# Optimization experiments

Hardware: AMD Instinct MI355X
Metric: run time of the kernel (lower is better)

Reference implementation:

```python
import jax, jax.numpy as jnp
import numpy as np
import math

B, S, D, H, DK, FF, L = 4, 1024, 512, 8, 64, 2048, 4
IN, NS, SD, TOPK = 768, 4, 64, 2


def _ln(x, g, b, eps=1e-5):
    mu = jnp.mean(x, -1, keepdims=True)
    var = jnp.mean((x - mu) ** 2, -1, keepdims=True)
    return (x - mu) / jnp.sqrt(var + eps) * g + b


def _pos_emb(s, d):
    pos = jnp.arange(s, dtype=jnp.float32)[:, None]
    div = jnp.exp(jnp.arange(0, d, 2, dtype=jnp.float32) * (-math.log(10000.0) / d))
    pe = jnp.zeros((s, d), jnp.float32)
    pe = pe.at[:, 0::2].set(jnp.sin(pos * div))
    pe = pe.at[:, 1::2].set(jnp.cos(pos * div))
    return pe


def setup_inputs() -> dict:
    key = jax.random.key(0)
    ks = iter(jax.random.split(key, 40))
    r = lambda *sh: jax.random.normal(next(ks), sh, jnp.float32)
    p = lambda *sh: jax.random.normal(next(ks), sh, jnp.float32) * 0.02
    inp = {
        'q_raw_seq': r(B, S, NS, IN),
        'm_seq': r(B, S, SD),
        'qa_embed': r(B, S, D),
        # MoE expert FFNs: Linear(IN,IN) -> ReLU -> Linear(IN,D)
        'exp_w1': p(NS, IN, IN), 'exp_b1': jnp.zeros((NS, IN)),
        'exp_w2': p(NS, IN, D), 'exp_b2': jnp.zeros((NS, D)),
        # router input adapter Linear(NS*IN, D)
        'adapt_w': p(NS * IN, D), 'adapt_b': jnp.zeros((D,)),
        'gate_w': p(D + SD, NS), 'gate_b': jnp.zeros((NS,)),
        'moe_ln_g': jnp.ones((D,)), 'moe_ln_b': jnp.zeros((D,)),
        # transformer blocks (kq_same=1 -> k_linear shared for q and k)
        'kw': p(L, D, D), 'kb': jnp.zeros((L, D)),
        'vw': p(L, D, D), 'vb': jnp.zeros((L, D)),
        'ow': p(L, D, D), 'ob': jnp.zeros((L, D)),
        'ln1_g': jnp.ones((L, D)), 'ln1_b': jnp.zeros((L, D)),
        'ff_w1': p(L, D, FF), 'ff_b1': jnp.zeros((L, FF)),
        'ff_w2': p(L, FF, D), 'ff_b2': jnp.zeros((L, D)),
        'ln2_g': jnp.ones((L, D)), 'ln2_b': jnp.zeros((L, D)),
    }
    return inp


def _forward(q_raw_seq, m_seq, qa_embed, exp_w1, exp_b1, exp_w2, exp_b2,
             adapt_w, adapt_b, gate_w, gate_b, moe_ln_g, moe_ln_b,
             kw, kb, vw, vb, ow, ob, ln1_g, ln1_b,
             ff_w1, ff_b1, ff_w2, ff_b2, ln2_g, ln2_b):
    # ---- PolyaParallelMoE (eval: no noise/dropout), has_stages=True ----
    h1 = jax.nn.relu(jnp.einsum('bske,kef->bskf', q_raw_seq, exp_w1) + exp_b1[None, None])
    experts = jnp.einsum('bskf,kfm->bskm', h1, exp_w2) + exp_b2[None, None]  # [B,S,4,D]
    q_flat = q_raw_seq.reshape(q_raw_seq.shape[0], q_raw_seq.shape[1], NS * IN)
    summary = jax.nn.relu(q_flat @ adapt_w + adapt_b)
    logits = jnp.concatenate([summary, m_seq], -1) @ gate_w + gate_b  # [B,S,4]
    top_vals, _ = jax.lax.top_k(logits, TOPK)
    thresh = top_vals[..., -1:]
    masked = jnp.where(logits >= thresh, logits, -jnp.inf)  # scatter top-k, -inf elsewhere
    gate_weights = jax.nn.softmax(masked, -1)
    combined = jnp.einsum('bskm,bsk->bsm', experts, gate_weights)
    q_embed = _ln(combined, moe_ln_g, moe_ln_b)

    # ---- Architecture: positional add + causal transformer blocks ----
    pe = _pos_emb(S, D)
    x = q_embed + pe
    y = qa_embed + pe
    allow = jnp.tril(jnp.ones((S, S), bool), -1)  # strict lower: np.triu(k=0)==0
    scale = 1.0 / math.sqrt(DK)
    for i in range(L):
        kh = (x @ kw[i] + kb[i]).reshape(B, S, H, DK).transpose(0, 2, 1, 3)
        vh = (y @ vw[i] + vb[i]).reshape(B, S, H, DK).transpose(0, 2, 1, 3)
        # kq_same: q = k_linear(query), query==key==x -> qh == kh
        scores = jnp.einsum('bhid,bhjd->bhij', kh, kh) * scale
        scores = jnp.where(allow, scores, -1e32)
        attn = jax.nn.softmax(scores, -1)
        attn = attn.at[:, :, 0, :].set(0.0)  # zero_pad first query row
        ctx = jnp.einsum('bhij,bhjd->bhid', attn, vh).transpose(0, 2, 1, 3).reshape(B, S, D)
        x = _ln(x + (ctx @ ow[i] + ob[i]), ln1_g[i], ln1_b[i])
        ffn = jax.nn.relu(x @ ff_w1[i] + ff_b1[i]) @ ff_w2[i] + ff_b2[i]
        x = _ln(x + ffn, ln2_g[i], ln2_b[i])
        y = x  # after first block, value stream follows torch loop (values=y fixed)
        y = qa_embed + pe  # values stay qa stream per Architecture.forward
    return x


def reference(q_raw_seq, m_seq, qa_embed, exp_w1, exp_b1, exp_w2, exp_b2,
              adapt_w, adapt_b, gate_w, gate_b, moe_ln_g, moe_ln_b,
              kw, kb, vw, vb, ow, ob, ln1_g, ln1_b,
              ff_w1, ff_b1, ff_w2, ff_b2, ln2_g, ln2_b):
    # NOTE: in Architecture.forward, each block is called with query=x, key=x, values=y
    # where y = qa_embed + pe stays fixed across blocks.
    def fwd(*a):
        return _forward(*a)
    return fwd(q_raw_seq, m_seq, qa_embed, exp_w1, exp_b1, exp_w2, exp_b2,
               adapt_w, adapt_b, gate_w, gate_b, moe_ln_g, moe_ln_b,
               kw, kb, vw, vb, ow, ob, ln1_g, ln1_b,
               ff_w1, ff_b1, ff_w2, ff_b2, ln2_g, ln2_b)
```

## Files before the change

### kernel.cpp

```cpp
#include <hip/hip_runtime.h>
#include <hip/hip_bf16.h>

typedef unsigned short u16;
typedef __attribute__((ext_vector_type(8))) short short8;
typedef __attribute__((ext_vector_type(4))) float floatx4;

template <typename T> struct is_u16 { static constexpr bool v = false; };
template <> struct is_u16<u16> { static constexpr bool v = true; };

__device__ __forceinline__ float bf2f(u16 u) {
    unsigned x = (unsigned)u << 16;
    return __uint_as_float(x);
}
__device__ __forceinline__ u16 f2bf(float f) {
    unsigned x = __float_as_uint(f);
    unsigned r = (x + 0x7fffu + ((x >> 16) & 1u)) >> 16;
    return (u16)r;
}

__device__ __forceinline__ float wave_sum(float v) {
    #pragma unroll
    for (int off = 32; off; off >>= 1) v += __shfl_xor(v, off);
    return v;
}

__device__ __forceinline__ void async16(const u16* g, const u16* lds) {
    __builtin_amdgcn_global_load_lds(
        (const __attribute__((address_space(1))) void*)g,
        (__attribute__((address_space(3))) void*)lds, 16, 0, 0);
}

__device__ __forceinline__ void hilo8(const float* p, u16* hi, u16* lo) {
    float4 a = *(const float4*)p, b = *(const float4*)(p + 4);
    float v[8] = {a.x, a.y, a.z, a.w, b.x, b.y, b.z, b.w};
    #pragma unroll
    for (int i = 0; i < 8; ++i) {
        u16 h = f2bf(v[i]);
        hi[i] = h;
        lo[i] = f2bf(v[i] - bf2f(h));
    }
}

__global__ __launch_bounds__(256) void hilo_conv_kernel(
    const float* __restrict__ in, u16* __restrict__ hi, u16* __restrict__ lo)
{
    const size_t i = ((size_t)blockIdx.x * 256 + threadIdx.x) * 8;
    u16 h[8], l[8];
    hilo8(in + i, h, l);
    *(uint4*)&hi[i] = *(const uint4*)h;
    *(uint4*)&lo[i] = *(const uint4*)l;
}

__device__ __forceinline__ void gemm_body(
    const u16* __restrict__ A, int lda,
    const u16* __restrict__ Bt, int ldb,
    const float* __restrict__ bias,
    float* __restrict__ Cf, u16* __restrict__ Cb, int ldc,
    int K, int act, int transC, int m0, int n0)
{
    __shared__ __align__(16) u16 Asm[2 * 128 * 32];
    __shared__ __align__(16) u16 Bsm[2 * 128 * 32];

    const int tid = threadIdx.x;
    const int lane = tid & 63;
    const int wave = tid >> 6;
    const int wm = (wave >> 1) * 64, wn = (wave & 1) * 64;

    const int r0 = tid >> 2;
    const int kc = (tid & 3) * 8;

    const int kq = (lane >> 4) * 8;
    const int fm = lane & 15;

    const floatx4 zz = {0.f, 0.f, 0.f, 0.f};
    floatx4 acc[4][4];
    #pragma unroll
    for (int mt = 0; mt < 4; ++mt)
        #pragma unroll
        for (int nt = 0; nt < 4; ++nt) acc[mt][nt] = zz;

    const u16* ldsA = Asm + wave * 512;
    const u16* ldsB = Bsm + wave * 512;

    for (int kt = 0; kt < K; kt += 64) {
        #pragma unroll
        for (int h = 0; h < 2; ++h) {
            async16(&A[(size_t)(m0 + r0) * lda + kt + h * 32 + kc],      ldsA + h * 4096);
            async16(&A[(size_t)(m0 + r0 + 64) * lda + kt + h * 32 + kc], ldsA + h * 4096 + 2048);
            async16(&Bt[(size_t)(n0 + r0) * ldb + kt + h * 32 + kc],      ldsB + h * 4096);
            async16(&Bt[(size_t)(n0 + r0 + 64) * ldb + kt + h * 32 + kc], ldsB + h * 4096 + 2048);
        }
        __syncthreads();

        #pragma unroll
        for (int h = 0; h < 2; ++h) {
            short8 af[4], bfr[4];
            #pragma unroll
            for (int mt = 0; mt < 4; ++mt)
                af[mt] = *(const short8*)&Asm[h * 4096 + (wm + mt * 16 + fm) * 32 + kq];
            #pragma unroll
            for (int nt = 0; nt < 4; ++nt)
                bfr[nt] = *(const short8*)&Bsm[h * 4096 + (wn + nt * 16 + fm) * 32 + kq];

            #pragma unroll
            for (int mt = 0; mt < 4; ++mt)
                #pragma unroll
                for (int nt = 0; nt < 4; ++nt)
                    acc[mt][nt] = __builtin_amdgcn_mfma_f32_16x16x32_bf16(
                        af[mt], bfr[nt], acc[mt][nt], 0, 0, 0);
        }
        __syncthreads();
    }

    const int cr = (lane >> 4) * 4;
    #pragma unroll
    for (int mt = 0; mt < 4; ++mt) {
        #pragma unroll
        for (int nt = 0; nt < 4; ++nt) {
            const int col = n0 + wn + nt * 16 + fm;
            const float bz = bias ? bias[col] : 0.f;
            #pragma unroll
            for (int r = 0; r < 4; ++r) {
                const int row = m0 + wm + mt * 16 + cr + r;
                float v = acc[mt][nt][r] + bz;
                if (act) v = fmaxf(v, 0.f);
                if (Cf) Cf[(size_t)row * ldc + col] = v;
                if (Cb) {
                    if (transC)
                        Cb[(((size_t)(row >> 10) * 512 + col) << 10) + (row & 1023)] = f2bf(v);
                    else
                        Cb[(size_t)row * ldc + col] = f2bf(v);
                }
            }
        }
    }
}

template <typename TA>
__global__ __launch_bounds__(256) void gemm_bf16(
    const TA* __restrict__ A, int lda, long strideAz,
    const u16* __restrict__ Bt, int ldb, long strideBz,
    const float* __restrict__ bias, int strideBiasZ,
    float* __restrict__ Cf, u16* __restrict__ Cb, int ldc, long strideCz,
    int K, int act, int transC, int NT)
{
    const int wg   = blockIdx.x;
    const int xcd  = wg & 7;
    const int slot = wg >> 3;
    const int nt   = slot % NT;
    const int pg   = slot / NT;
    const int panel = xcd + 8 * pg;
    const int my = panel & 31, mz = panel >> 5;

    A  += (size_t)mz * strideAz;
    Bt += (size_t)mz * strideBz;
    const float* bz = bias ? bias + (size_t)mz * strideBiasZ : nullptr;
    if (Cf) Cf += (size_t)mz * strideCz;
    if (Cb) Cb += (size_t)mz * strideCz;
    gemm_body(A, lda, Bt, ldb, bz, Cf, Cb, ldc, K, act, transC, my * 128, nt * 128);
}

__global__ __launch_bounds__(256) void gemm_kv(
    const u16* __restrict__ xb, const u16* __restrict__ yb,
    const u16* __restrict__ kwt, const u16* __restrict__ vwt,
    const float* __restrict__ kb, const float* __restrict__ vb,
    u16* __restrict__ khb, u16* __restrict__ vhT)
{
    const int wg   = blockIdx.x;
    const int xcd  = wg & 7;
    const int slot = wg >> 3;
    const int nt   = slot & 3;
    const int pg   = slot >> 2;
    const int panel = xcd + 8 * pg;
    const int my = panel & 31, mz = panel >> 5;

    if (mz == 0)
        gemm_body(xb, 512, kwt, 512, kb, nullptr, khb, 512, 512, 0, 0, my * 128, nt * 128);
    else
        gemm_body(yb, 512, vwt, 512, vb, nullptr, vhT, 512, 512, 0, 1, my * 128, nt * 128);
}

__global__ __launch_bounds__(256) void gemm_f32split(
    const u16* __restrict__ Ah, const u16* __restrict__ Al, int lda,
    const u16* __restrict__ Bh, const u16* __restrict__ Bl, int ldb,
    float* __restrict__ Cf, int ldc, long strideCz,
    int kz)
{
    __shared__ __align__(16) u16 Ahs[2 * 128 * 32];
    __shared__ __align__(16) u16 Als[2 * 128 * 32];
    __shared__ __align__(16) u16 Bhs[2 * 128 * 32];
    __shared__ __align__(16) u16 Bls[2 * 128 * 32];

    const int wg   = blockIdx.x;
    const int xcd  = wg & 7;
    const int slot = wg >> 3;
    const int nt4  = slot & 3;
    const int g    = xcd + 8 * (slot >> 2);
    const int my   = g & 31, mz = g >> 5;

    const int tid = threadIdx.x;
    const int lane = tid & 63;
    const int wave = tid >> 6;
    const int m0 = my * 128, n0 = nt4 * 128;
    const int wm = (wave >> 1) * 64, wn = (wave & 1) * 64;
    const int k0 = mz * kz;
    Cf += (size_t)mz * strideCz;

    const int r0 = tid >> 2;
    const int kc = (tid & 3) * 8;
    const int kq = (lane >> 4) * 8;
    const int fm = lane & 15;

    const floatx4 zz = {0.f, 0.f, 0.f, 0.f};
    floatx4 acc[4][4];
    #pragma unroll
    for (int mt = 0; mt < 4; ++mt)
        #pragma unroll
        for (int nt = 0; nt < 4; ++nt) acc[mt][nt] = zz;

    const u16* ldsAh = Ahs + wave * 512;
    const u16* ldsAl = Als + wave * 512;
    const u16* ldsBh = Bhs + wave * 512;
    const u16* ldsBl = Bls + wave * 512;

    for (int kt = 0; kt < kz; kt += 64) {
        #pragma unroll
        for (int h = 0; h < 2; ++h) {
            const size_t ka = (size_t)(m0 + r0) * lda + k0 + kt + h * 32 + kc;
            const size_t kb = (size_t)(n0 + r0) * ldb + k0 + kt + h * 32 + kc;
            async16(&Ah[ka],                     ldsAh + h * 4096);
            async16(&Ah[ka + (size_t)64 * lda],  ldsAh + h * 4096 + 2048);
            async16(&Al[ka],                     ldsAl + h * 4096);
            async16(&Al[ka + (size_t)64 * lda],  ldsAl + h * 4096 + 2048);
            async16(&Bh[kb],                     ldsBh + h * 4096);
            async16(&Bh[kb + (size_t)64 * ldb],  ldsBh + h * 4096 + 2048);
            async16(&Bl[kb],                     ldsBl + h * 4096);
            async16(&Bl[kb + (size_t)64 * ldb],  ldsBl + h * 4096 + 2048);
        }
        __syncthreads();

        #pragma unroll
        for (int h = 0; h < 2; ++h) {
            short8 ah[4], al[4], bh[4], bl[4];
            #pragma unroll
            for (int mt = 0; mt < 4; ++mt) {
                ah[mt] = *(const short8*)&Ahs[h * 4096 + (wm + mt * 16 + fm) * 32 + kq];
                al[mt] = *(const short8*)&Als[h * 4096 + (wm + mt * 16 + fm) * 32 + kq];
            }
            #pragma unroll
            for (int nt = 0; nt < 4; ++nt) {
                bh[nt] = *(const short8*)&Bhs[h * 4096 + (wn + nt * 16 + fm) * 32 + kq];
                bl[nt] = *(const short8*)&Bls[h * 4096 + (wn + nt * 16 + fm) * 32 + kq];
            }

            #pragma unroll
            for (int mt = 0; mt < 4; ++mt)
                #pragma unroll
                for (int nt = 0; nt < 4; ++nt) {
                    acc[mt][nt] = __builtin_amdgcn_mfma_f32_16x16x32_bf16(
                        ah[mt], bh[nt], acc[mt][nt], 0, 0, 0);
                    acc[mt][nt] = __builtin_amdgcn_mfma_f32_16x16x32_bf16(
                        al[mt], bh[nt], acc[mt][nt], 0, 0, 0);
                    acc[mt][nt] = __builtin_amdgcn_mfma_f32_16x16x32_bf16(
                        ah[mt], bl[nt], acc[mt][nt], 0, 0, 0);
                }
        }
        __syncthreads();
    }

    const int cr = (lane >> 4) * 4;
    #pragma unroll
    for (int mt = 0; mt < 4; ++mt) {
        #pragma unroll
        for (int nt = 0; nt < 4; ++nt) {
            const int col = n0 + wn + nt * 16 + fm;
            #pragma unroll
            for (int r = 0; r < 4; ++r) {
                const int row = m0 + wm + mt * 16 + cr + r;
                Cf[(size_t)row * ldc + col] = acc[mt][nt][r];
            }
        }
    }
}

__global__ __launch_bounds__(64) void gate_fused_kernel(
    const float* __restrict__ ps, const float* __restrict__ adapt_b,
    const float* __restrict__ m_seq,
    const float* __restrict__ gw, const float* __restrict__ gb,
    float* __restrict__ gates)
{
    const int r = blockIdx.x, t = threadIdx.x;
    float p0 = 0.f, p1 = 0.f, p2 = 0.f, p3 = 0.f;
    const float* pr = ps + (size_t)r * 512;
    for (int j = t; j < 512; j += 64) {
        float v = pr[j] + pr[j + 2097152] + pr[j + 4194304] + pr[j + 6291456] + adapt_b[j];
        float s = fmaxf(v, 0.f);
        const float* g = gw + (size_t)j * 4;
        p0 += s * g[0]; p1 += s * g[1]; p2 += s * g[2]; p3 += s * g[3];
    }
    {
        float m = m_seq[(size_t)r * 64 + t];
        const float* g = gw + (size_t)(512 + t) * 4;
        p0 += m * g[0]; p1 += m * g[1]; p2 += m * g[2]; p3 += m * g[3];
    }
    p0 = wave_sum(p0); p1 = wave_sum(p1); p2 = wave_sum(p2); p3 = wave_sum(p3);
    if (t == 0) {
        float lg[4] = { p0 + gb[0], p1 + gb[1], p2 + gb[2], p3 + gb[3] };
        float m1 = -INFINITY, m2 = -INFINITY;
        #pragma unroll
        for (int k = 0; k < 4; ++k) {
            float v = lg[k];
            if (v > m1) { m2 = m1; m1 = v; }
            else if (v > m2) { m2 = v; }
        }
        float wv[4], s = 0.f;
        #pragma unroll
        for (int k = 0; k < 4; ++k) {
            wv[k] = (lg[k] >= m2) ? __expf(lg[k] - m1) : 0.f;
            s += wv[k];
        }
        float inv = 1.f / s;
        #pragma unroll
        for (int k = 0; k < 4; ++k) gates[(size_t)r * 4 + k] = wv[k] * inv;
    }
}

__global__ __launch_bounds__(256) void tconv_kernel(
    const float* __restrict__ in, u16* __restrict__ out, int K, int N)
{
    __shared__ float t[32][33];
    const int n0 = blockIdx.x * 32, k0 = blockIdx.y * 32;
    const size_t bo = (size_t)blockIdx.z * K * N;
    const int tx = threadIdx.x & 31, ty = threadIdx.x >> 5;
    const float* src = in + bo;
    u16* dst = out + bo;
    #pragma unroll
    for (int r = ty; r < 32; r += 8) t[r][tx] = src[(size_t)(k0 + r) * N + n0 + tx];
    __syncthreads();
    #pragma unroll
    for (int r = ty; r < 32; r += 8) dst[(size_t)(n0 + r) * K + k0 + tx] = f2bf(t[tx][r]);
}

__global__ __launch_bounds__(256) void tconv3_kernel(
    const float* __restrict__ kw, const float* __restrict__ vw, const float* __restrict__ ow,
    u16* __restrict__ kwt, u16* __restrict__ vwt, u16* __restrict__ owt)
{
    __shared__ float t[32][33];
    const int z = blockIdx.z;
    const int sel = z >> 2, li = z & 3;
    const float* in = (sel == 0) ? kw : (sel == 1) ? vw : ow;
    u16* outp = (sel == 0) ? kwt : (sel == 1) ? vwt : owt;
    const size_t bo = (size_t)li * 262144;
    const int n0 = blockIdx.x * 32, k0 = blockIdx.y * 32;
    const int tx = threadIdx.x & 31, ty = threadIdx.x >> 5;
    const float* src = in + bo;
    u16* dst = outp + bo;
    #pragma unroll
    for (int r = ty; r < 32; r += 8) t[r][tx] = src[(size_t)(k0 + r) * 512 + n0 + tx];
    __syncthreads();
    #pragma unroll
    for (int r = ty; r < 32; r += 8) dst[(size_t)(n0 + r) * 512 + k0 + tx] = f2bf(t[tx][r]);
}

__global__ __launch_bounds__(256) void tconv_hilo_kernel(
    const float* __restrict__ in, u16* __restrict__ outh, u16* __restrict__ outl,
    int K, int N)
{
    __shared__ float t[32][33];
    const int n0 = blockIdx.x * 32, k0 = blockIdx.y * 32;
    const int tx = threadIdx.x & 31, ty = threadIdx.x >> 5;
    #pragma unroll
    for (int r = ty; r < 32; r += 8) t[r][tx] = in[(size_t)(k0 + r) * N + n0 + tx];
    __syncthreads();
    #pragma unroll
    for (int r = ty; r < 32; r += 8) {
        float v = t[tx][r];
        u16 h = f2bf(v);
        outh[(size_t)(n0 + r) * K + k0 + tx] = h;
        outl[(size_t)(n0 + r) * K + k0 + tx] = f2bf(v - bf2f(h));
    }
}

__global__ void pe_kernel(float* __restrict__ pe)
{
    int idx = blockIdx.x * 256 + threadIdx.x;
    int s = idx >> 9, d = idx & 511;
    float div = expf((float)(d & ~1) * (-9.210340371976184f / 512.0f));
    float ang = (float)s * div;
    pe[idx] = (d & 1) ? cosf(ang) : sinf(ang);
}

__global__ __launch_bounds__(64) void moe_ln_kernel(
    const u16* __restrict__ experts, const float* __restrict__ gates,
    const float* __restrict__ g, const float* __restrict__ bb,
    const float* __restrict__ pe, const float* __restrict__ qa,
    float* __restrict__ x, u16* __restrict__ xb, u16* __restrict__ yb)
{
    const int r = blockIdx.x, t = threadIdx.x;
    const u16* e = experts + (size_t)r * 2048;
    const float g0 = gates[r * 4 + 0], g1 = gates[r * 4 + 1];
    const float g2 = gates[r * 4 + 2], g3 = gates[r * 4 + 3];
    float v[8];
    #pragma unroll
    for (int it = 0; it < 8; ++it) {
        int d = t + it * 64;
        v[it] = g0 * bf2f(e[d]) + g1 * bf2f(e[512 + d])
              + g2 * bf2f(e[1024 + d]) + g3 * bf2f(e[1536 + d]);
    }
    float s = 0.f;
    #pragma unroll
    for (int it = 0; it < 8; ++it) s += v[it];
    s = wave_sum(s);
    const float mu = s * (1.f / 512.f);
    float q = 0.f;
    #pragma unroll
    for (int it = 0; it < 8; ++it) { float dd = v[it] - mu; q += dd * dd; }
    q = wave_sum(q);
    const float rstd = rsqrtf(q * (1.f / 512.f) + 1e-5f);
    const float* per = pe + (size_t)(r & 1023) * 512;
    #pragma unroll
    for (int it = 0; it < 8; ++it) {
        int d = t + it * 64;
        float pv = per[d];
        float o = (v[it] - mu) * rstd * g[d] + bb[d] + pv;
        x[(size_t)r * 512 + d] = o;
        xb[(size_t)r * 512 + d] = f2bf(o);
        yb[(size_t)r * 512 + d] = f2bf(qa[(size_t)r * 512 + d] + pv);
    }
}

__global__ __launch_bounds__(64) void add_ln_kernel(
    float* __restrict__ x, u16* __restrict__ xb,
    const float* __restrict__ t0, const float* __restrict__ t1,
    const float* __restrict__ bias,
    const float* __restrict__ g, const float* __restrict__ bb,
    float* __restrict__ out2)
{
    const int r = blockIdx.x, t = threadIdx.x;
    float* xr = x + (size_t)r * 512;
    float v[8];
    #pragma unroll
    for (int it = 0; it < 8; ++it) {
        int d = t + it * 64;
        float tv = t0[(size_t)r * 512 + d];
        if (t1) tv += t1[(size_t)r * 512 + d];
        if (bias) tv += bias[d];
        v[it] = xr[d] + tv;
    }
    float s = 0.f;
    #pragma unroll
    for (int it = 0; it < 8; ++it) s += v[it];
    s = wave_sum(s);
    const float mu = s * (1.f / 512.f);
    float q = 0.f;
    #pragma unroll
    for (int it = 0; it < 8; ++it) { float dd = v[it] - mu; q += dd * dd; }
    q = wave_sum(q);
    const float rstd = rsqrtf(q * (1.f / 512.f) + 1e-5f);
    #pragma unroll
    for (int it = 0; it < 8; ++it) {
        int d = t + it * 64;
        float o = (v[it] - mu) * rstd * g[d] + bb[d];
        xr[d] = o;
        xb[(size_t)r * 512 + d] = f2bf(o);
        if (out2) out2[(size_t)r * 512 + d] = o;
    }
}

__global__ __launch_bounds__(256) void attn_kernel(
    const u16* __restrict__ kh, const u16* __restrict__ vhT,
    u16* __restrict__ ctx)
{
    __shared__ __align__(16) u16 Qs[64 * 64];
    __shared__ __align__(16) u16 Ks[64 * 64];
    __shared__ __align__(16) u16 Vt[64 * 72];
    __shared__ __align__(16) u16 Ps[64 * 72];

    const int tid = threadIdx.x;
    const int lane = tid & 63, wave = tid >> 6;
    const int quad = lane >> 4, fm = lane & 15;
    const int b = blockIdx.x, h = blockIdx.y;
    const int bz = blockIdx.z;
    const int it = (bz < 8) ? bz : (23 - bz);

    const u16* khb = kh + ((size_t)b * 1024) * 512 + h * 64;
    const u16* vtb = vhT + ((size_t)(b * 512 + h * 64)) * 1024;

    const int lj = tid >> 2;
    const int lc = tid & 3;

    {
        const u16* src = khb + (size_t)(it * 64 + lj) * 512 + lc * 16;
        *(uint4*)&Qs[lj * 64 + lc * 16]     = *(const uint4*)src;
        *(uint4*)&Qs[lj * 64 + lc * 16 + 8] = *(const uint4*)(src + 8);
    }

    const floatx4 zz = {0.f, 0.f, 0.f, 0.f};
    floatx4 o_acc[4];
    #pragma unroll
    for (int nt = 0; nt < 4; ++nt) o_acc[nt] = zz;
    float m_run[4] = { -INFINITY, -INFINITY, -INFINITY, -INFINITY };
    float l_run[4] = {};

    __syncthreads();

    for (int jt = 0; jt <= it; ++jt) {
        {
            const u16* ksrc = khb + (size_t)(jt * 64 + lj) * 512 + lc * 16;
            *(uint4*)&Ks[lj * 64 + lc * 16]     = *(const uint4*)ksrc;
            *(uint4*)&Ks[lj * 64 + lc * 16 + 8] = *(const uint4*)(ksrc + 8);
            const u16* vsrc = vtb + (size_t)lj * 1024 + jt * 64 + lc * 16;
            *(uint4*)&Vt[lj * 72 + lc * 16]     = *(const uint4*)vsrc;
            *(uint4*)&Vt[lj * 72 + lc * 16 + 8] = *(const uint4*)(vsrc + 8);
        }
        __syncthreads();

        floatx4 s_acc[4];
        #pragma unroll
        for (int nt = 0; nt < 4; ++nt) s_acc[nt] = zz;
        #pragma unroll
        for (int ks = 0; ks < 2; ++ks) {
            short8 af = *(const short8*)&Qs[(wave * 16 + fm) * 64 + ks * 32 + quad * 8];
            #pragma unroll
            for (int nt = 0; nt < 4; ++nt) {
                short8 bf = *(const short8*)&Ks[(nt * 16 + fm) * 64 + ks * 32 + quad * 8];
                s_acc[nt] = __builtin_amdgcn_mfma_f32_16x16x32_bf16(af, bf, s_acc[nt], 0, 0, 0);
            }
        }

        const bool diag = (jt == it);
        #pragma unroll
        for (int r = 0; r < 4; ++r) {
            const int rowi = wave * 16 + quad * 4 + r;
            float sv[4];
            #pragma unroll
            for (int nt = 0; nt < 4; ++nt) {
                float s = s_acc[nt][r] * 0.125f;
                if (diag && (nt * 16 + fm) >= rowi) s = -INFINITY;
                sv[nt] = s;
            }
            float mx = fmaxf(fmaxf(sv[0], sv[1]), fmaxf(sv[2], sv[3]));
            #pragma unroll
            for (int off = 1; off < 16; off <<= 1) mx = fmaxf(mx, __shfl_xor(mx, off));
            const float mn = fmaxf(m_run[r], mx);
            const float mfix = (mn == -INFINITY) ? 0.f : mn;
            const float alpha = (m_run[r] == -INFINITY) ? 0.f : __expf(m_run[r] - mn);
            m_run[r] = mn;
            float rs = 0.f;
            #pragma unroll
            for (int nt = 0; nt < 4; ++nt) {
                float p = __expf(sv[nt] - mfix);
                Ps[rowi * 72 + nt * 16 + fm] = f2bf(p);
                rs += p;
            }
            #pragma unroll
            for (int off = 1; off < 16; off <<= 1) rs += __shfl_xor(rs, off);
            l_run[r] = l_run[r] * alpha + rs;
            #pragma unroll
            for (int nt = 0; nt < 4; ++nt) o_acc[nt][r] *= alpha;
        }
        __syncthreads();

        #pragma unroll
        for (int ks = 0; ks < 2; ++ks) {
            short8 af = *(const short8*)&Ps[(wave * 16 + fm) * 72 + ks * 32 + quad * 8];
            #pragma unroll
            for (int nt = 0; nt < 4; ++nt) {
                short8 bf = *(const short8*)&Vt[(nt * 16 + fm) * 72 + ks * 32 + quad * 8];
                o_acc[nt] = __builtin_amdgcn_mfma_f32_16x16x32_bf16(af, bf, o_acc[nt], 0, 0, 0);
            }
        }
        __syncthreads();
    }

    u16* cb = ctx + ((size_t)b * 1024 + (size_t)it * 64 + wave * 16) * 512 + h * 64;
    #pragma unroll
    for (int r = 0; r < 4; ++r) {
        const int row = quad * 4 + r;
        const float inv = (l_run[r] > 0.f) ? 1.f / l_run[r] : 0.f;
        #pragma unroll
        for (int nt = 0; nt < 4; ++nt)
            cb[(size_t)row * 512 + nt * 16 + fm] = f2bf(o_acc[nt][r] * inv);
    }
}

extern "C" void kernel_launch(void* const* d_in, const int* in_sizes, int n_in,
                              void* d_out, int out_size, void* d_ws, size_t ws_size,
                              hipStream_t stream)
{
    const float* q_raw   = (const float*)d_in[0];
    const float* m_seq   = (const float*)d_in[1];
    const float* qa      = (const float*)d_in[2];
    const float* exp_w1  = (const float*)d_in[3];
    const float* exp_b1  = (const float*)d_in[4];
    const float* exp_w2  = (const float*)d_in[5];
    const float* exp_b2  = (const float*)d_in[6];
    const float* adapt_w = (const float*)d_in[7];
    const float* adapt_b = (const float*)d_in[8];
    const float* gate_w  = (const float*)d_in[9];
    const float* gate_b  = (const float*)d_in[10];
    const float* moe_g   = (const float*)d_in[11];
    const float* moe_b   = (const float*)d_in[12];
    const float* kw      = (const float*)d_in[13];
    const float* kb      = (const float*)d_in[14];
    const float* vw      = (const float*)d_in[15];
    const float* vb      = (const float*)d_in[16];
    const float* ow      = (const float*)d_in[17];
    const float* ob      = (const float*)d_in[18];
    const float* ln1g    = (const float*)d_in[19];
    const float* ln1b    = (const float*)d_in[20];
    const float* fw1     = (const float*)d_in[21];
    const float* fb1     = (const float*)d_in[22];
    const float* fw2     = (const float*)d_in[23];
    const float* fb2     = (const float*)d_in[24];
    const float* ln2g    = (const float*)d_in[25];
    const float* ln2b    = (const float*)d_in[26];
    float* out = (float*)d_out;

    const size_t NEED = 125829120ull;
    if (ws_size < NEED) return;

    char* base = (char*)d_ws;
    float* x  = (float*)(base + 0);
    u16*  xb  = (u16*)(base + 8388608);
    u16*  yb  = (u16*)(base + 12582912);
    char* G = base + 16777216;
    u16*   w1t     = (u16*)(G + 0);
    u16*   w2t     = (u16*)(G + 4718592);
    float* psum    = (float*)(G + 7864320);
    u16*   h1b4    = (u16*)(G + 7864320);
    u16*   expb    = (u16*)(G + 33030144);
    float* pe      = (float*)(G + 49807360);
    float* gates   = (float*)(G + 51904512);
    u16*   adwh    = (u16*)(G + 52428800);
    u16*   adwl    = (u16*)(G + 55574528);
    u16*   qhi     = (u16*)(G + 58720256);
    u16*   qlo     = (u16*)(G + 83886080);
    u16*   kwt  = (u16*)(G + 0);
    u16*   vwt  = (u16*)(G + 2097152);
    u16*   owt  = (u16*)(G + 4194304);
    u16*   fw1t = (u16*)(G + 6291456);
    u16*   fw2t = (u16*)(G + 14680064);
    u16*   khb  = (u16*)(G + 23068672);
    u16*   vhT  = (u16*)(G + 27262976);
    u16*   ctxb = (u16*)(G + 31457280);
    float* p    = (float*)(G + 35651584);
    u16*   ffhb = (u16*)(G + 44040192);
    float* ps0  = (float*)(G + 23068672);

    pe_kernel<<<2048, 256, 0, stream>>>(pe);
    hilo_conv_kernel<<<6144, 256, 0, stream>>>(q_raw, qhi, qlo);
    tconv_kernel<<<dim3(24, 24, 4), 256, 0, stream>>>(exp_w1, w1t, 768, 768);
    tconv_kernel<<<dim3(16, 24, 4), 256, 0, stream>>>(exp_w2, w2t, 768, 512);
    tconv_hilo_kernel<<<dim3(16, 96), 256, 0, stream>>>(adapt_w, adwh, adwl, 3072, 512);

    gemm_f32split<<<512, 256, 0, stream>>>(
        qhi, qlo, 3072, adwh, adwl, 3072, psum, 512, 2097152L, 768);
    gate_fused_kernel<<<4096, 64, 0, stream>>>(
        psum, adapt_b, m_seq, gate_w, gate_b, gates);

    gemm_bf16<u16><<<768, 256, 0, stream>>>(
        qhi, 3072, 768L, w1t, 768, 589824L, exp_b1, 768,
        nullptr, h1b4, 768, 3145728L, 768, 1, 0, 6);
    gemm_bf16<u16><<<512, 256, 0, stream>>>(
        h1b4, 768, 3145728L, w2t, 768, 393216L, exp_b2, 512,
        nullptr, expb, 2048, 512L, 768, 0, 0, 4);
    moe_ln_kernel<<<4096, 64, 0, stream>>>(expb, gates, moe_g, moe_b, pe, qa, x, xb, yb);

    tconv3_kernel<<<dim3(16, 16, 12), 256, 0, stream>>>(kw, vw, ow, kwt, vwt, owt);
    tconv_kernel<<<dim3(64, 16, 4), 256, 0, stream>>>(fw1, fw1t, 512, 2048);
    tconv_kernel<<<dim3(16, 64, 4), 256, 0, stream>>>(fw2, fw2t, 2048, 512);

    for (int i = 0; i < 4; ++i) {
        gemm_kv<<<256, 256, 0, stream>>>(
            xb, yb, kwt + (size_t)i * 262144, vwt + (size_t)i * 262144,
            kb + i * 512, vb + i * 512, khb, vhT);
        attn_kernel<<<dim3(4, 8, 16), 256, 0, stream>>>(khb, vhT, ctxb);
        gemm_bf16<u16><<<128, 256, 0, stream>>>(
            ctxb, 512, 0L, owt + (size_t)i * 262144, 512, 0L, ob + i * 512, 0,
            p, nullptr, 512, 0L, 512, 0, 0, 4);
        add_ln_kernel<<<4096, 64, 0, stream>>>(
            x, xb, p, nullptr, nullptr, ln1g + i * 512, ln1b + i * 512, nullptr);
        gemm_bf16<u16><<<512, 256, 0, stream>>>(
            xb, 512, 0L, fw1t + (size_t)i * 1048576, 512, 0L, fb1 + i * 2048, 0,
            nullptr, ffhb, 2048, 0L, 512, 1, 0, 16);
        gemm_bf16<u16><<<256, 256, 0, stream>>>(
            ffhb, 2048, 1024L, fw2t + (size_t)i * 1048576, 2048, 1024L, nullptr, 0,
            ps0, nullptr, 512, 2097152L, 1024, 0, 0, 4);
        add_ln_kernel<<<4096, 64, 0, stream>>>(
            x, xb, ps0, ps0 + 2097152, fb2 + i * 512,
            ln2g + i * 512, ln2b + i * 512, (i == 3) ? out : nullptr);
    }
}
```

Before: 889.4 us.

## Double-buffer LDS tiles in GEMMs and attention to overlap loads with MFMA

The bf16 GEMM body, the hi/lo split fp32 GEMM and the causal attention kernel now double-buffer their shared-memory tiles. The next K-tile (or next K/V block) is prefetched while MFMAs run on the current one, and one barrier per iteration is dropped. In attention, K/V for the next block are loaded into registers early and written to the alternate buffer after the PV product. This targets global-load latency that was exposed between barriers. The cost is more LDS: the GEMM body's shared memory doubles to 64KB, which may lower occupancy, and the split GEMM moves to a 32-wide K step.

```diff
diff --git a/kernel.cpp b/kernel.cpp
--- a/kernel.cpp
+++ b/kernel.cpp
@@ -4,9 +4,6 @@
 typedef unsigned short u16;
 typedef __attribute__((ext_vector_type(8))) short short8;
 typedef __attribute__((ext_vector_type(4))) float floatx4;
-
-template <typename T> struct is_u16 { static constexpr bool v = false; };
-template <> struct is_u16<u16> { static constexpr bool v = true; };
 
 __device__ __forceinline__ float bf2f(u16 u) {
     unsigned x = (unsigned)u << 16;
@@ -58,8 +55,8 @@
     float* __restrict__ Cf, u16* __restrict__ Cb, int ldc,
     int K, int act, int transC, int m0, int n0)
 {
-    __shared__ __align__(16) u16 Asm[2 * 128 * 32];
-    __shared__ __align__(16) u16 Bsm[2 * 128 * 32];
+    __shared__ __align__(16) u16 Asm[2][8192];
+    __shared__ __align__(16) u16 Bsm[2][8192];
 
     const int tid = threadIdx.x;
     const int lane = tid & 63;
@@ -68,7 +65,6 @@
 
     const int r0 = tid >> 2;
     const int kc = (tid & 3) * 8;
-
     const int kq = (lane >> 4) * 8;
     const int fm = lane & 15;
 
@@ -79,28 +75,33 @@
         #pragma unroll
         for (int nt = 0; nt < 4; ++nt) acc[mt][nt] = zz;
 
-    const u16* ldsA = Asm + wave * 512;
-    const u16* ldsB = Bsm + wave * 512;
+    auto stage = [&](int kt, int b) {
+        #pragma unroll
+        for (int h = 0; h < 2; ++h) {
+            async16(&A[(size_t)(m0 + r0) * lda + kt + h * 32 + kc],      &Asm[b][h * 4096 + wave * 512]);
+            async16(&A[(size_t)(m0 + r0 + 64) * lda + kt + h * 32 + kc], &Asm[b][h * 4096 + 2048 + wave * 512]);
+            async16(&Bt[(size_t)(n0 + r0) * ldb + kt + h * 32 + kc],      &Bsm[b][h * 4096 + wave * 512]);
+            async16(&Bt[(size_t)(n0 + r0 + 64) * ldb + kt + h * 32 + kc], &Bsm[b][h * 4096 + 2048 + wave * 512]);
+        }
+    };
+
+    stage(0, 0);
+    __syncthreads();
 
     for (int kt = 0; kt < K; kt += 64) {
-        #pragma unroll
-        for (int h = 0; h < 2; ++h) {
-            async16(&A[(size_t)(m0 + r0) * lda + kt + h * 32 + kc],      ldsA + h * 4096);
-            async16(&A[(size_t)(m0 + r0 + 64) * lda + kt + h * 32 + kc], ldsA + h * 4096 + 2048);
-            async16(&Bt[(size_t)(n0 + r0) * ldb + kt + h * 32 + kc],      ldsB + h * 4096);
-            async16(&Bt[(size_t)(n0 + r0 + 64) * ldb + kt + h * 32 + kc], ldsB + h * 4096 + 2048);
-        }
-        __syncthreads();
+        const int cur = (kt >> 6) & 1;
+        const bool more = (kt + 64 < K);
+        if (more) stage(kt + 64, cur ^ 1);
 
         #pragma unroll
         for (int h = 0; h < 2; ++h) {
             short8 af[4], bfr[4];
             #pragma unroll
             for (int mt = 0; mt < 4; ++mt)
-                af[mt] = *(const short8*)&Asm[h * 4096 + (wm + mt * 16 + fm) * 32 + kq];
+                af[mt] = *(const short8*)&Asm[cur][h * 4096 + (wm + mt * 16 + fm) * 32 + kq];
             #pragma unroll
             for (int nt = 0; nt < 4; ++nt)
-                bfr[nt] = *(const short8*)&Bsm[h * 4096 + (wn + nt * 16 + fm) * 32 + kq];
+                bfr[nt] = *(const short8*)&Bsm[cur][h * 4096 + (wn + nt * 16 + fm) * 32 + kq];
 
             #pragma unroll
             for (int mt = 0; mt < 4; ++mt)
@@ -109,7 +110,7 @@
                     acc[mt][nt] = __builtin_amdgcn_mfma_f32_16x16x32_bf16(
                         af[mt], bfr[nt], acc[mt][nt], 0, 0, 0);
         }
-        __syncthreads();
+        if (more) __syncthreads();
     }
 
     const int cr = (lane >> 4) * 4;
@@ -186,10 +187,10 @@
     float* __restrict__ Cf, int ldc, long strideCz,
     int kz)
 {
-    __shared__ __align__(16) u16 Ahs[2 * 128 * 32];
-    __shared__ __align__(16) u16 Als[2 * 128 * 32];
-    __shared__ __align__(16) u16 Bhs[2 * 128 * 32];
-    __shared__ __align__(16) u16 Bls[2 * 128 * 32];
+    __shared__ __align__(16) u16 Ahs[2][4096];
+    __shared__ __align__(16) u16 Als[2][4096];
+    __shared__ __align__(16) u16 Bhs[2][4096];
+    __shared__ __align__(16) u16 Bls[2][4096];
 
     const int wg   = blockIdx.x;
     const int xcd  = wg & 7;
@@ -218,54 +219,51 @@
         #pragma unroll
         for (int nt = 0; nt < 4; ++nt) acc[mt][nt] = zz;
 
-    const u16* ldsAh = Ahs + wave * 512;
-    const u16* ldsAl = Als + wave * 512;
-    const u16* ldsBh = Bhs + wave * 512;
-    const u16* ldsBl = Bls + wave * 512;
-
-    for (int kt = 0; kt < kz; kt += 64) {
-        #pragma unroll
-        for (int h = 0; h < 2; ++h) {
-            const size_t ka = (size_t)(m0 + r0) * lda + k0 + kt + h * 32 + kc;
-            const size_t kb = (size_t)(n0 + r0) * ldb + k0 + kt + h * 32 + kc;
-            async16(&Ah[ka],                     ldsAh + h * 4096);
-            async16(&Ah[ka + (size_t)64 * lda],  ldsAh + h * 4096 + 2048);
-            async16(&Al[ka],                     ldsAl + h * 4096);
-            async16(&Al[ka + (size_t)64 * lda],  ldsAl + h * 4096 + 2048);
-            async16(&Bh[kb],                     ldsBh + h * 4096);
-            async16(&Bh[kb + (size_t)64 * ldb],  ldsBh + h * 4096 + 2048);
-            async16(&Bl[kb],                     ldsBl + h * 4096);
-            async16(&Bl[kb + (size_t)64 * ldb],  ldsBl + h * 4096 + 2048);
-        }
-        __syncthreads();
-
-        #pragma unroll
-        for (int h = 0; h < 2; ++h) {
-            short8 ah[4], al[4], bh[4], bl[4];
-            #pragma unroll
-            for (int mt = 0; mt < 4; ++mt) {
-                ah[mt] = *(const short8*)&Ahs[h * 4096 + (wm + mt * 16 + fm) * 32 + kq];
-                al[mt] = *(const short8*)&Als[h * 4096 + (wm + mt * 16 + fm) * 32 + kq];
+    auto stage = [&](int kt, int b) {
+        const size_t ka = (size_t)(m0 + r0) * lda + k0 + kt + kc;
+        const size_t kb = (size_t)(n0 + r0) * ldb + k0 + kt + kc;
+        async16(&Ah[ka],                    &Ahs[b][wave * 512]);
+        async16(&Ah[ka + (size_t)64 * lda], &Ahs[b][2048 + wave * 512]);
+        async16(&Al[ka],                    &Als[b][wave * 512]);
+        async16(&Al[ka + (size_t)64 * lda], &Als[b][2048 + wave * 512]);
+        async16(&Bh[kb],                    &Bhs[b][wave * 512]);
+        async16(&Bh[kb + (size_t)64 * ldb], &Bhs[b][2048 + wave * 512]);
+        async16(&Bl[kb],                    &Bls[b][wave * 512]);
+        async16(&Bl[kb + (size_t)64 * ldb], &Bls[b][2048 + wave * 512]);
+    };
+
+    stage(0, 0);
+    __syncthreads();
+
+    for (int kt = 0; kt < kz; kt += 32) {
+        const int cur = (kt >> 5) & 1;
+        const bool more = (kt + 32 < kz);
+        if (more) stage(kt + 32, cur ^ 1);
+
+        short8 ah[4], al[4], bh[4], bl[4];
+        #pragma unroll
+        for (int mt = 0; mt < 4; ++mt) {
+            ah[mt] = *(const short8*)&Ahs[cur][(wm + mt * 16 + fm) * 32 + kq];
+            al[mt] = *(const short8*)&Als[cur][(wm + mt * 16 + fm) * 32 + kq];
+        }
+        #pragma unroll
+        for (int nt = 0; nt < 4; ++nt) {
+            bh[nt] = *(const short8*)&Bhs[cur][(wn + nt * 16 + fm) * 32 + kq];
+            bl[nt] = *(const short8*)&Bls[cur][(wn + nt * 16 + fm) * 32 + kq];
+        }
+
+        #pragma unroll
+        for (int mt = 0; mt < 4; ++mt)
+            #pragma unroll
+            for (int nt = 0; nt < 4; ++nt) {
+                acc[mt][nt] = __builtin_amdgcn_mfma_f32_16x16x32_bf16(
+                    ah[mt], bh[nt], acc[mt][nt], 0, 0, 0);
+                acc[mt][nt] = __builtin_amdgcn_mfma_f32_16x16x32_bf16(
+                    al[mt], bh[nt], acc[mt][nt], 0, 0, 0);
+                acc[mt][nt] = __builtin_amdgcn_mfma_f32_16x16x32_bf16(
+                    ah[mt], bl[nt], acc[mt][nt], 0, 0, 0);
             }
-            #pragma unroll
-            for (int nt = 0; nt < 4; ++nt) {
-                bh[nt] = *(const short8*)&Bhs[h * 4096 + (wn + nt * 16 + fm) * 32 + kq];
-                bl[nt] = *(const short8*)&Bls[h * 4096 + (wn + nt * 16 + fm) * 32 + kq];
-            }
-
-            #pragma unroll
-            for (int mt = 0; mt < 4; ++mt)
-                #pragma unroll
-                for (int nt = 0; nt < 4; ++nt) {
-                    acc[mt][nt] = __builtin_amdgcn_mfma_f32_16x16x32_bf16(
-                        ah[mt], bh[nt], acc[mt][nt], 0, 0, 0);
-                    acc[mt][nt] = __builtin_amdgcn_mfma_f32_16x16x32_bf16(
-                        al[mt], bh[nt], acc[mt][nt], 0, 0, 0);
-                    acc[mt][nt] = __builtin_amdgcn_mfma_f32_16x16x32_bf16(
-                        ah[mt], bl[nt], acc[mt][nt], 0, 0, 0);
-                }
-        }
-        __syncthreads();
+        if (more) __syncthreads();
     }
 
     const int cr = (lane >> 4) * 4;
@@ -472,8 +470,8 @@
     u16* __restrict__ ctx)
 {
     __shared__ __align__(16) u16 Qs[64 * 64];
-    __shared__ __align__(16) u16 Ks[64 * 64];
-    __shared__ __align__(16) u16 Vt[64 * 72];
+    __shared__ __align__(16) u16 Ks[2][64 * 64];
+    __shared__ __align__(16) u16 Vt[2][64 * 72];
     __shared__ __align__(16) u16 Ps[64 * 72];
 
     const int tid = threadIdx.x;
@@ -495,6 +493,15 @@
         *(uint4*)&Qs[lj * 64 + lc * 16 + 8] = *(const uint4*)(src + 8);
     }
 
+    {
+        const u16* ksrc = khb + (size_t)(lj) * 512 + lc * 16;
+        *(uint4*)&Ks[0][lj * 64 + lc * 16]     = *(const uint4*)ksrc;
+        *(uint4*)&Ks[0][lj * 64 + lc * 16 + 8] = *(const uint4*)(ksrc + 8);
+        const u16* vsrc = vtb + (size_t)lj * 1024 + lc * 16;
+        *(uint4*)&Vt[0][lj * 72 + lc * 16]     = *(const uint4*)vsrc;
+        *(uint4*)&Vt[0][lj * 72 + lc * 16 + 8] = *(const uint4*)(vsrc + 8);
+    }
+
     const floatx4 zz = {0.f, 0.f, 0.f, 0.f};
     floatx4 o_acc[4];
     #pragma unroll
@@ -505,15 +512,18 @@
     __syncthreads();
 
     for (int jt = 0; jt <= it; ++jt) {
-        {
-            const u16* ksrc = khb + (size_t)(jt * 64 + lj) * 512 + lc * 16;
-            *(uint4*)&Ks[lj * 64 + lc * 16]     = *(const uint4*)ksrc;
-            *(uint4*)&Ks[lj * 64 + lc * 16 + 8] = *(const uint4*)(ksrc + 8);
-            const u16* vsrc = vtb + (size_t)lj * 1024 + jt * 64 + lc * 16;
-            *(uint4*)&Vt[lj * 72 + lc * 16]     = *(const uint4*)vsrc;
-            *(uint4*)&Vt[lj * 72 + lc * 16 + 8] = *(const uint4*)(vsrc + 8);
-        }
-        __syncthreads();
+        const int cur = jt & 1;
+        const bool pf = (jt < it);
+
+        uint4 kr0, kr1, vr0, vr1;
+        if (pf) {
+            const u16* ksrc = khb + (size_t)((jt + 1) * 64 + lj) * 512 + lc * 16;
+            kr0 = *(const uint4*)ksrc;
+            kr1 = *(const uint4*)(ksrc + 8);
+            const u16* vsrc = vtb + (size_t)lj * 1024 + (jt + 1) * 64 + lc * 16;
+            vr0 = *(const uint4*)vsrc;
+            vr1 = *(const uint4*)(vsrc + 8);
+        }
 
         floatx4 s_acc[4];
         #pragma unroll
@@ -523,7 +533,7 @@
             short8 af = *(const short8*)&Qs[(wave * 16 + fm) * 64 + ks * 32 + quad * 8];
             #pragma unroll
             for (int nt = 0; nt < 4; ++nt) {
-                short8 bf = *(const short8*)&Ks[(nt * 16 + fm) * 64 + ks * 32 + quad * 8];
+                short8 bf = *(const short8*)&Ks[cur][(nt * 16 + fm) * 64 + ks * 32 + quad * 8];
                 s_acc[nt] = __builtin_amdgcn_mfma_f32_16x16x32_bf16(af, bf, s_acc[nt], 0, 0, 0);
             }
         }
@@ -559,18 +569,24 @@
             #pragma unroll
             for (int nt = 0; nt < 4; ++nt) o_acc[nt][r] *= alpha;
         }
-        __syncthreads();
 
         #pragma unroll
         for (int ks = 0; ks < 2; ++ks) {
             short8 af = *(const short8*)&Ps[(wave * 16 + fm) * 72 + ks * 32 + quad * 8];
             #pragma unroll
             for (int nt = 0; nt < 4; ++nt) {
-                short8 bf = *(const short8*)&Vt[(nt * 16 + fm) * 72 + ks * 32 + quad * 8];
+                short8 bf = *(const short8*)&Vt[cur][(nt * 16 + fm) * 72 + ks * 32 + quad * 8];
                 o_acc[nt] = __builtin_amdgcn_mfma_f32_16x16x32_bf16(af, bf, o_acc[nt], 0, 0, 0);
             }
         }
-        __syncthreads();
+
+        if (pf) {
+            *(uint4*)&Ks[cur ^ 1][lj * 64 + lc * 16]     = kr0;
+            *(uint4*)&Ks[cur ^ 1][lj * 64 + lc * 16 + 8] = kr1;
+            *(uint4*)&Vt[cur ^ 1][lj * 72 + lc * 16]     = vr0;
+            *(uint4*)&Vt[cur ^ 1][lj * 72 + lc * 16 + 8] = vr1;
+            __syncthreads();
+        }
     }
 
     u16* cb = ctx + ((size_t)b * 1024 + (size_t)it * 64 + wave * 16) * 512 + h * 64;
```

Result: no change. 905.7 us (+1.8%).
